# Kernel optimization log

Hardware: AMD Instinct MI355X
Metric: run time of the kernel (lower is better)

Reference implementation:

```python
import jax, jax.numpy as jnp
import numpy as np

SLOPE = 0.01

def leaky_tanh(x):
    return jnp.tanh(x * (2.0 / 3.0)) * 1.7159 + x * SLOPE

def lstm_cell(x, h, c, w_ih, w_hh, b_ih, b_hh):
    # torch LSTMCell gate order: i, f, g, o
    gates = x @ w_ih.T + b_ih + h @ w_hh.T + b_hh
    i, f, g, o = jnp.split(gates, 4, axis=-1)
    c_new = jax.nn.sigmoid(f) * c + jax.nn.sigmoid(i) * jnp.tanh(g)
    h_new = jax.nn.sigmoid(o) * jnp.tanh(c_new)
    return h_new, c_new

def setup_inputs() -> dict:
    key = jax.random.key(0)
    ks = jax.random.split(key, 16)
    T, B, I, H, O = 512, 64, 128, 2048, 64
    H1, H2 = H // 2, H // 8  # 1024, 256
    F2 = H // 4              # 512
    s = 0.02
    return {
        "inputs": jax.random.normal(ks[0], (T, B, I), dtype=jnp.float32),
        "fc1_w": jax.random.normal(ks[1], (H, I), dtype=jnp.float32) * s,
        "fc1_b": jax.random.normal(ks[2], (H,), dtype=jnp.float32) * s,
        "w_ih1": jax.random.normal(ks[3], (4 * H1, H), dtype=jnp.float32) * s,
        "w_hh1": jax.random.normal(ks[4], (4 * H1, H1), dtype=jnp.float32) * s,
        "b_ih1": jax.random.normal(ks[5], (4 * H1,), dtype=jnp.float32) * s,
        "b_hh1": jax.random.normal(ks[6], (4 * H1,), dtype=jnp.float32) * s,
        "fc2_w": jax.random.normal(ks[7], (F2, H1), dtype=jnp.float32) * s,
        "fc2_b": jax.random.normal(ks[8], (F2,), dtype=jnp.float32) * s,
        "w_ih2": jax.random.normal(ks[9], (4 * H2, F2), dtype=jnp.float32) * s,
        "w_hh2": jax.random.normal(ks[10], (4 * H2, H2), dtype=jnp.float32) * s,
        "b_ih2": jax.random.normal(ks[11], (4 * H2,), dtype=jnp.float32) * s,
        "b_hh2": jax.random.normal(ks[12], (4 * H2,), dtype=jnp.float32) * s,
        "fc3_w": jax.random.normal(ks[13], (O, H2), dtype=jnp.float32) * s,
        "fc3_b": jax.random.normal(ks[14], (O,), dtype=jnp.float32) * s,
    }

def reference(inputs, fc1_w, fc1_b, w_ih1, w_hh1, b_ih1, b_hh1,
              fc2_w, fc2_b, w_ih2, w_hh2, b_ih2, b_hh2, fc3_w, fc3_b):
    T, B, _ = inputs.shape
    H1 = w_hh1.shape[1]
    H2 = w_hh2.shape[1]
    h1 = jnp.zeros((B, H1), dtype=inputs.dtype)
    c1 = jnp.zeros((B, H1), dtype=inputs.dtype)
    h2 = jnp.zeros((B, H2), dtype=inputs.dtype)
    c2 = jnp.zeros((B, H2), dtype=inputs.dtype)

    def step(carry, xt):
        h1, c1, h2, c2 = carry
        x = leaky_tanh(xt @ fc1_w.T + fc1_b)
        h1, c1 = lstm_cell(x, h1, c1, w_ih1, w_hh1, b_ih1, b_hh1)
        x = leaky_tanh(h1 @ fc2_w.T + fc2_b)
        h2, c2 = lstm_cell(x, h2, c2, w_ih2, w_hh2, b_ih2, b_hh2)
        yhat = h2 @ fc3_w.T + fc3_b
        return (h1, c1, h2, c2), yhat

    _, outputs = jax.lax.scan(step, (h1, c1, h2, c2), inputs)
    return outputs  # [T, B, output_size]
```

## Files before the change

kernel.cpp:

```cpp
#include <hip/hip_runtime.h>
#include <hip/hip_bf16.h>

static constexpr int T_  = 512;
static constexpr int B_  = 64;
static constexpr int I_  = 128;
static constexpr int H_  = 2048;
static constexpr int H1_ = 1024;
static constexpr int F2_ = 512;
static constexpr int H2_ = 256;
static constexpr int O_  = 64;
static constexpr int G1N = 4096;
static constexpr int G2N = 1024;
static constexpr int NW  = 176;

typedef __attribute__((ext_vector_type(8))) __bf16 bfx8;
typedef __attribute__((ext_vector_type(4))) __bf16 bfx4;
typedef __attribute__((ext_vector_type(4))) float  fx4;

#define DEV __device__ __forceinline__

DEV fx4 mfma16(bfx8 a, bfx8 b, fx4 c) {
  return __builtin_amdgcn_mfma_f32_16x16x32_bf16(a, b, c, 0, 0, 0);
}
DEV float fast_sig(float x) { return 1.0f / (1.0f + __expf(-x)); }
DEV float fast_tanh(float x) {
  x = fminf(fmaxf(x, -30.0f), 30.0f);
  return 2.0f / (1.0f + __expf(-2.0f * x)) - 1.0f;
}
DEV float leaky_tanh_(float x) { return fast_tanh(x * (2.0f / 3.0f)) * 1.7159f + 0.01f * x; }

DEV void gld16c(const void* g, void* l) {
  __builtin_amdgcn_global_load_lds(
      (const __attribute__((address_space(1))) unsigned int*)g,
      (__attribute__((address_space(3))) unsigned int*)l, 16, 0, 17);
}
DEV void spin_ge(int* p, int tgt) {
  while (__hip_atomic_load(p, __ATOMIC_RELAXED, __HIP_MEMORY_SCOPE_AGENT) < tgt)
    __builtin_amdgcn_s_sleep(1);
}
DEV void stc2(unsigned short* p, unsigned short v) {
  __hip_atomic_store(p, v, __ATOMIC_RELAXED, __HIP_MEMORY_SCOPE_AGENT);
}
DEV unsigned long long ldc8(const void* p) {
  return __hip_atomic_load((const unsigned long long*)p, __ATOMIC_RELAXED,
                           __HIP_MEMORY_SCOPE_AGENT);
}
DEV unsigned short bf16bits(float f) {
  __bf16 h = (__bf16)f;
  return __builtin_bit_cast(unsigned short, h);
}
DEV void arrive1(int* p) {
  __hip_atomic_fetch_add(p, 1, __ATOMIC_RELAXED, __HIP_MEMORY_SCOPE_AGENT);
}

__global__ void k_f2b(const float* __restrict__ s, __bf16* __restrict__ d, int n4) {
  int i = blockIdx.x * blockDim.x + threadIdx.x;
  int st = gridDim.x * blockDim.x;
  for (; i < n4; i += st) {
    float4 v = ((const float4*)s)[i];
    bfx4 o = { (__bf16)v.x, (__bf16)v.y, (__bf16)v.z, (__bf16)v.w };
    ((bfx4*)d)[i] = o;
  }
}
__global__ void k_add2(const float* __restrict__ a, const float* __restrict__ b,
                       float* __restrict__ d, int n) {
  int i = blockIdx.x * blockDim.x + threadIdx.x;
  if (i < n) d[i] = a[i] + b[i];
}

__global__ void k_wre1(const float* __restrict__ w, __bf16* __restrict__ W2) {
  int v = blockIdx.x * 256 + threadIdx.x;
  int l = v & 63, kk = (v >> 6) & 31, g = (v >> 11) & 3, ng = v >> 13;
  int row = g * 1024 + ng * 16 + (l & 15);
  int k0  = kk * 32 + (l >> 4) * 8;
  const float* sp = w + (size_t)row * 1024 + k0;
  float4 v0 = ((const float4*)sp)[0];
  float4 v1 = ((const float4*)sp)[1];
  bfx8 o = { (__bf16)v0.x, (__bf16)v0.y, (__bf16)v0.z, (__bf16)v0.w,
             (__bf16)v1.x, (__bf16)v1.y, (__bf16)v1.z, (__bf16)v1.w };
  *(bfx8*)(W2 + (size_t)v * 8) = o;
}

DEV void gemm_tile(char* sm, const __bf16* __restrict__ A, const __bf16* __restrict__ W,
                   __bf16* __restrict__ outB, const float* __restrict__ bias,
                   int m0, int n0, int N, int K, int epi, int wt)
{
  __bf16 (*As)[32] = (__bf16 (*)[32])sm;
  __bf16 (*Ws)[32] = (__bf16 (*)[32])(sm + 8192);
  const int tid = threadIdx.x, lane = tid & 63, wave = tid >> 6;
  const int wm = wave >> 1, wn = wave & 1;
  const int r1 = tid >> 2, c1v = (tid & 3) * 8;
  const int kr = (lane >> 4) * 8, rr = lane & 15;
  fx4 acc[4][4] = {};
  for (int k0 = 0; k0 < K; k0 += 32) {
    __syncthreads();
    *(bfx8*)&As[r1][c1v]      = *(const bfx8*)&A[(size_t)(m0 + r1) * K + k0 + c1v];
    *(bfx8*)&As[r1 + 64][c1v] = *(const bfx8*)&A[(size_t)(m0 + r1 + 64) * K + k0 + c1v];
    *(bfx8*)&Ws[r1][c1v]      = *(const bfx8*)&W[(size_t)(n0 + r1) * K + k0 + c1v];
    *(bfx8*)&Ws[r1 + 64][c1v] = *(const bfx8*)&W[(size_t)(n0 + r1 + 64) * K + k0 + c1v];
    __syncthreads();
    bfx8 a[4], b[4];
#pragma unroll
    for (int mi = 0; mi < 4; ++mi) a[mi] = *(const bfx8*)&As[wm*64 + mi*16 + rr][kr];
#pragma unroll
    for (int ni = 0; ni < 4; ++ni) b[ni] = *(const bfx8*)&Ws[wn*64 + ni*16 + rr][kr];
#pragma unroll
    for (int mi = 0; mi < 4; ++mi)
#pragma unroll
      for (int ni = 0; ni < 4; ++ni)
        acc[mi][ni] = mfma16(a[mi], b[ni], acc[mi][ni]);
  }
  const int cr = (lane >> 4) * 4, cc = lane & 15;
#pragma unroll
  for (int mi = 0; mi < 4; ++mi)
#pragma unroll
    for (int ni = 0; ni < 4; ++ni) {
      int col = n0 + wn*64 + ni*16 + cc;
#pragma unroll
      for (int r = 0; r < 4; ++r) {
        int row = m0 + wm*64 + mi*16 + cr + r;
        float v = acc[mi][ni][r] + bias[col];
        if (epi == 1) v = leaky_tanh_(v);
        if (wt) stc2((unsigned short*)outB + ((size_t)row * N + col), bf16bits(v));
        else    outB[(size_t)row * N + col] = (__bf16)v;
      }
    }
}

__launch_bounds__(256)
__global__ void k_gemm(const __bf16* __restrict__ A, const __bf16* __restrict__ W,
                       __bf16* __restrict__ outB, const float* __restrict__ bias,
                       int M, int N, int K, int epi)
{
  __shared__ __align__(16) char sm[16384];
  (void)M;
  gemm_tile(sm, A, W, outB, bias, blockIdx.y * 128, blockIdx.x * 128, N, K, epi, 0);
}

DEV void stage(char* dst, int rsB, const __bf16* __restrict__ src, size_t sStride,
               int n, int lg) {
  for (int idx = threadIdx.x; idx < n; idx += 256) {
    int r = idx >> lg, c = idx & ((1 << lg) - 1);
    *(bfx8*)(dst + r * rsB + ((c * 16) ^ ((r & 7) << 4))) =
        *(const bfx8*)(src + (size_t)r * sStride + c * 8);
  }
}

struct KP {
  const __bf16 *W2, *whh2b;
  const __bf16 *g1rd;  __bf16 *g1wr;
  const __bf16 *xcrd;  __bf16 *xcwr;
  const __bf16 *infc1;
  const __bf16 *h1rd;  const __bf16 *h1s0;  __bf16 *h1wr;
  __bf16 *x2c; __bf16 *g2;
  const __bf16 *wfc1, *wih1, *wfc2, *wih2;
  const float *bfc1, *bs1, *bfc2, *bs2;
  float *c1, *c2;
  __bf16 *h2a;
  int *cnt;
  int Tc, t2base, do_l1, do_l2, do_fc2, do_ih1, do_fc1;
};

__launch_bounds__(256, 1)
__global__ void k_persist3(KP p)
{
  __shared__ __align__(16) char smem[131072];
  const int tid = threadIdx.x, lane = tid & 63, wv = tid >> 6;
  const int rr = lane & 15, hi = lane >> 4;
  const int col = tid & 15, brow = tid >> 4;
  const int bid = blockIdx.x;
  int* cnt = p.cnt;
  const int Tc = p.Tc;

  if (bid < 64) {
    if (!p.do_l1) return;
    const int ng = bid;
    char* As = smem;
    float* Cp = (float*)smem;

    bfx8 wreg[4][8];
#pragma unroll
    for (int g = 0; g < 4; ++g)
#pragma unroll
      for (int j = 0; j < 8; ++j)
        wreg[g][j] = *(const bfx8*)(p.W2 + (size_t)((ng * 4 + g) * 32 + wv * 8 + j) * 512 + lane * 8);

    float pc[4];
#pragma unroll
    for (int q = 0; q < 4; ++q)
      pc[q] = p.c1[(brow + q * 16) * 1024 + ng * 16 + col];

    for (int s = 0; s < Tc; ++s) {
      float pg[4][4];
#pragma unroll
      for (int q = 0; q < 4; ++q)
#pragma unroll
        for (int g = 0; g < 4; ++g)
          pg[q][g] = (float)p.g1rd[(size_t)(s * 64 + brow + q * 16) * 4096 + g * 1024 + ng * 16 + col];

      if (s > 0 && tid < 4) spin_ge(cnt + tid * 128, 16 * s);
      __syncthreads();

      const __bf16* h1s = (s == 0) ? p.h1s0 : (p.h1wr + (size_t)s * 65536);
      {
        char* dstb = smem + wv * 32768;
#pragma unroll 8
        for (int i = 0; i < 32; ++i) {
          int d = wv * 2048 + i * 64 + lane;
          int r = d >> 7;
          int sg = (r << 7) | ((d & 127) ^ (r & 7));
          gld16c(h1s + (size_t)sg * 8, dstb + i * 1024);
        }
      }
      __syncthreads();

      fx4 acc[4][4] = {};
#pragma unroll
      for (int j = 0; j < 8; ++j) {
        const int kB = (wv * 8 + j) * 64 + hi * 16;
        bfx8 a[4];
#pragma unroll
        for (int m = 0; m < 4; ++m) {
          int ra = m * 16 + rr;
          a[m] = *(const bfx8*)(As + ra * 2048 + (kB ^ ((ra & 7) << 4)));
        }
#pragma unroll
        for (int g = 0; g < 4; ++g)
#pragma unroll
          for (int m = 0; m < 4; ++m)
            acc[g][m] = mfma16(a[m], wreg[g][j], acc[g][m]);
      }
      __syncthreads();
#pragma unroll
      for (int g = 0; g < 4; ++g)
#pragma unroll
        for (int m = 0; m < 4; ++m) {
          int gc = g * 16 + rr;
          int bx = (m * 16 + hi * 4) ^ ((gc & 15) << 2);
          *(fx4*)(Cp + ((wv * 64 + gc) * 64 + bx)) = acc[g][m];
        }
      __syncthreads();

      __bf16* h1o = p.h1wr + (size_t)(s + 1) * 65536;
#pragma unroll
      for (int q = 0; q < 4; ++q) {
        int b_ = brow + q * 16;
        float gv[4];
#pragma unroll
        for (int g = 0; g < 4; ++g) {
          int gc = g * 16 + col;
          int bx = b_ ^ ((gc & 15) << 2);
          float v = pg[q][g];
#pragma unroll
          for (int w = 0; w < 4; ++w)
            v += Cp[(w * 64 + gc) * 64 + bx];
          gv[g] = v;
        }
        float cn = fast_sig(gv[1]) * pc[q] + fast_sig(gv[0]) * fast_tanh(gv[2]);
        pc[q] = cn;
        float hv = fast_sig(gv[3]) * fast_tanh(cn);
        stc2((unsigned short*)h1o + (b_ * 1024 + ng * 16 + col), bf16bits(hv));
      }
      __syncthreads();
      if (tid == 0) arrive1(cnt + (ng & 3) * 128);
    }
#pragma unroll
    for (int q = 0; q < 4; ++q)
      p.c1[(brow + q * 16) * 1024 + ng * 16 + col] = pc[q];

  } else if (bid < 80) {
    if (!p.do_l2) return;
    const int ng2 = bid - 64;
    char* Ws2 = smem;
    char* As2 = smem + 32768;
    float (*Gx2)[64][16] = (float (*)[64][16])(smem + 32768);

    for (int idx = tid; idx < 2048; idx += 256) {
      int r = idx >> 5, c = idx & 31;
      int wr = (r >> 4) * 256 + ng2 * 16 + (r & 15);
      *(bfx8*)(Ws2 + r * 512 + ((c * 16) ^ ((r & 7) << 4))) =
          *(const bfx8*)(p.whh2b + (size_t)wr * 256 + c * 8);
    }
    float pc2[4];
#pragma unroll
    for (int q = 0; q < 4; ++q)
      pc2[q] = p.c2[(brow + q * 16) * 256 + ng2 * 16 + col];

    if (tid == 0) spin_ge(cnt + 640, NW);
    __syncthreads();

    for (int s = 0; s < Tc; ++s) {
      float pg[4][4];
#pragma unroll
      for (int q = 0; q < 4; ++q)
#pragma unroll
        for (int g = 0; g < 4; ++g)
          pg[q][g] = (float)p.g2[(size_t)(s * 64 + brow + q * 16) * 1024 + g * 256 + ng2 * 16 + col];

      if (s > 0 && tid == 0) spin_ge(cnt + 512, 16 * s);
      __syncthreads();

      const __bf16* h2s = p.h2a + (size_t)(p.t2base + s) * 16384;
      for (int idx = tid; idx < 2048; idx += 256) {
        int r = idx >> 5, c = idx & 31;
        const char* sp = (const char*)(h2s + r * 256 + c * 8);
        unsigned long long lo = ldc8(sp), hi8 = ldc8(sp + 8);
        char* dp = As2 + r * 512 + ((c * 16) ^ ((r & 7) << 4));
        *(unsigned long long*)dp = lo;
        *(unsigned long long*)(dp + 8) = hi8;
      }
      __syncthreads();

      fx4 acc[4] = {};
#pragma unroll
      for (int ks = 0; ks < 8; ++ks) {
        const int cb = ks * 64 + hi * 16;
        int rb = wv * 16 + rr;
        bfx8 bfr = *(const bfx8*)(Ws2 + rb * 512 + (cb ^ ((rb & 7) << 4)));
#pragma unroll
        for (int m = 0; m < 4; ++m) {
          int ra = m * 16 + rr;
          bfx8 afr = *(const bfx8*)(As2 + ra * 512 + (cb ^ ((ra & 7) << 4)));
          acc[m] = mfma16(afr, bfr, acc[m]);
        }
      }
      __syncthreads();
#pragma unroll
      for (int m = 0; m < 4; ++m)
#pragma unroll
        for (int r = 0; r < 4; ++r)
          Gx2[wv][m * 16 + hi * 4 + r][rr] = acc[m][r];
      __syncthreads();

      __bf16* h2o = p.h2a + (size_t)(p.t2base + s + 1) * 16384;
#pragma unroll
      for (int q = 0; q < 4; ++q) {
        int b_ = brow + q * 16;
        float gi = Gx2[0][b_][col] + pg[q][0];
        float gf = Gx2[1][b_][col] + pg[q][1];
        float gg = Gx2[2][b_][col] + pg[q][2];
        float go = Gx2[3][b_][col] + pg[q][3];
        float cn = fast_sig(gf) * pc2[q] + fast_sig(gi) * fast_tanh(gg);
        pc2[q] = cn;
        float hv = fast_sig(go) * fast_tanh(cn);
        stc2((unsigned short*)h2o + (b_ * 256 + ng2 * 16 + col), bf16bits(hv));
      }
      __syncthreads();
      if (tid == 0) arrive1(cnt + 512);
    }
#pragma unroll
    for (int q = 0; q < 4; ++q)
      p.c2[(brow + q * 16) * 256 + ng2 * 16 + col] = pc2[q];

  } else {
    const int wid = bid - 80;
    const int Mt = (Tc * 64) / 128;
    if (p.do_fc2) {
      for (int i = wid; i < Mt * 4; i += NW)
        gemm_tile(smem, p.h1rd + 65536, p.wfc2, p.x2c, p.bfc2,
                  (i >> 2) * 128, (i & 3) * 128, F2_, H1_, 1, 1);
      __syncthreads();
      if (tid == 0) { arrive1(cnt + 576); spin_ge(cnt + 576, NW); }
      __syncthreads();
      for (int i = wid; i < Mt * 8; i += NW)
        gemm_tile(smem, p.x2c, p.wih2, p.g2, p.bs2,
                  (i >> 3) * 128, (i & 7) * 128, G2N, F2_, 0, 1);
      __syncthreads();
      if (tid == 0) arrive1(cnt + 640);
    }
    if (p.do_ih1) {
      for (int i = wid; i < Mt * 32; i += NW)
        gemm_tile(smem, p.xcrd, p.wih1, p.g1wr, p.bs1,
                  (i >> 5) * 128, (i & 31) * 128, G1N, H_, 0, 0);
    }
    if (p.do_fc1) {
      for (int i = wid; i < Mt * 16; i += NW)
        gemm_tile(smem, p.infc1, p.wfc1, p.xcwr, p.bfc1,
                  (i >> 4) * 128, (i & 15) * 128, H_, I_, 1, 0);
    }
  }
}

__launch_bounds__(256)
__global__ void k_fc3b(const __bf16* __restrict__ H2mat, const __bf16* __restrict__ w3,
                       const float* __restrict__ b3, float* __restrict__ out)
{
  __shared__ __align__(16) char smem[65536];
  const int tid = threadIdx.x, lane = tid & 63, wv = tid >> 6;
  const int rr = lane & 15, hi = lane >> 4;
  char* As = smem;
  char* Ws = smem + 32768;
  const size_t row0 = (size_t)blockIdx.x * 64;
  stage(As, 512, H2mat + row0 * 256, 256, 2048, 5);
  stage(Ws, 512, w3, 256, 2048, 5);
  __syncthreads();
  fx4 acc[4] = {};
#pragma unroll
  for (int ks = 0; ks < 8; ++ks) {
    const int cbB = ks * 64 + hi * 16;
    int rb = wv * 16 + rr;
    bfx8 bfr = *(const bfx8*)(Ws + rb * 512 + (cbB ^ ((rb & 7) << 4)));
#pragma unroll
    for (int m = 0; m < 4; ++m) {
      int ra = m * 16 + rr;
      bfx8 afr = *(const bfx8*)(As + ra * 512 + (cbB ^ ((ra & 7) << 4)));
      acc[m] = mfma16(afr, bfr, acc[m]);
    }
  }
  float bv = b3[wv * 16 + rr];
#pragma unroll
  for (int m = 0; m < 4; ++m)
#pragma unroll
    for (int r = 0; r < 4; ++r)
      out[(row0 + m * 16 + hi * 4 + r) * 64 + wv * 16 + rr] = acc[m][r] + bv;
}

extern "C" void kernel_launch(void* const* d_in, const int* in_sizes, int n_in,
                              void* d_out, int out_size, void* d_ws, size_t ws_size,
                              hipStream_t stream)
{
  (void)in_sizes; (void)n_in; (void)out_size;
  const float* f_in = (const float*)d_in[0];
  const float* fc1w = (const float*)d_in[1];
  const float* fc1b = (const float*)d_in[2];
  const float* wih1 = (const float*)d_in[3];
  const float* whh1 = (const float*)d_in[4];
  const float* bih1 = (const float*)d_in[5];
  const float* bhh1 = (const float*)d_in[6];
  const float* fc2w = (const float*)d_in[7];
  const float* fc2b = (const float*)d_in[8];
  const float* wih2 = (const float*)d_in[9];
  const float* whh2 = (const float*)d_in[10];
  const float* bih2 = (const float*)d_in[11];
  const float* bhh2 = (const float*)d_in[12];
  const float* fc3w = (const float*)d_in[13];
  const float* fc3b = (const float*)d_in[14];
  float* out = (float*)d_out;

  char* base = (char*)d_ws;
  size_t off = 0;
  auto alloc = [&](size_t bytes) -> char* {
    char* q = base + off;
    off = (off + bytes + 255) & ~(size_t)255;
    return q;
  };
  __bf16* wb_fc1 = (__bf16*)alloc((size_t)H_ * I_ * 2);
  __bf16* wb_ih1 = (__bf16*)alloc((size_t)G1N * H_ * 2);
  __bf16* W2     = (__bf16*)alloc((size_t)G1N * H1_ * 2);
  __bf16* wb_fc2 = (__bf16*)alloc((size_t)F2_ * H1_ * 2);
  __bf16* wb_ih2 = (__bf16*)alloc((size_t)G2N * F2_ * 2);
  __bf16* wb_hh2 = (__bf16*)alloc((size_t)G2N * H2_ * 2);
  __bf16* wb_fc3 = (__bf16*)alloc((size_t)O_ * H2_ * 2);
  __bf16* in_bf  = (__bf16*)alloc((size_t)T_ * B_ * I_ * 2);
  float*  bsum1  = (float*) alloc((size_t)G1N * 4);
  float*  bsum2  = (float*) alloc((size_t)G2N * 4);
  float*  c1     = (float*) alloc((size_t)B_ * H1_ * 4);
  float*  c2     = (float*) alloc((size_t)B_ * H2_ * 4);
  __bf16* h2a    = (__bf16*)alloc((size_t)(T_ + 1) * B_ * H2_ * 2);
  __bf16* h1zero = (__bf16*)alloc((size_t)B_ * H1_ * 2);
  int*    cnt    = (int*)   alloc(4096);
  size_t fixed = off;

  auto perTc = [](size_t Tc) -> size_t {
    size_t Mc = Tc * 64;
    return 2 * Mc * H_ * 2
         + 2 * Mc * G1N * 2
         + 2 * (Tc + 1) * (size_t)B_ * H1_ * 2
         + Mc * F2_ * 2
         + Mc * G2N * 2
         + 10 * 256;
  };
  int Tc = 128;
  while (Tc > 2 && fixed + perTc(Tc) > ws_size) Tc >>= 1;
  const int Mc = Tc * 64;
  __bf16* XcA  = (__bf16*)alloc((size_t)Mc * H_ * 2);
  __bf16* XcB  = (__bf16*)alloc((size_t)Mc * H_ * 2);
  __bf16* G1A  = (__bf16*)alloc((size_t)Mc * G1N * 2);
  __bf16* G1B  = (__bf16*)alloc((size_t)Mc * G1N * 2);
  __bf16* h1rA = (__bf16*)alloc((size_t)(Tc + 1) * B_ * H1_ * 2);
  __bf16* h1rB = (__bf16*)alloc((size_t)(Tc + 1) * B_ * H1_ * 2);
  __bf16* x2c  = (__bf16*)alloc((size_t)Mc * F2_ * 2);
  __bf16* G2cb = (__bf16*)alloc((size_t)Mc * G2N * 2);

  struct CV { const float* s; __bf16* d; int n; } cvs[7] = {
    {fc1w, wb_fc1, H_ * I_},   {wih1, wb_ih1, G1N * H_},
    {fc2w, wb_fc2, F2_ * H1_}, {wih2, wb_ih2, G2N * F2_}, {whh2, wb_hh2, G2N * H2_},
    {fc3w, wb_fc3, O_ * H2_},  {f_in, in_bf, T_ * B_ * I_},
  };
  for (int i = 0; i < 7; ++i) {
    int n4 = cvs[i].n / 4;
    int blocks = (n4 + 255) / 256;
    if (blocks > 2048) blocks = 2048;
    k_f2b<<<blocks, 256, 0, stream>>>(cvs[i].s, cvs[i].d, n4);
  }
  k_wre1<<<2048, 256, 0, stream>>>(whh1, W2);
  k_add2<<<G1N / 256, 256, 0, stream>>>(bih1, bhh1, bsum1, G1N);
  k_add2<<<G2N / 256, 256, 0, stream>>>(bih2, bhh2, bsum2, G2N);
  hipMemsetAsync(c1, 0, (size_t)B_ * H1_ * 4, stream);
  hipMemsetAsync(c2, 0, (size_t)B_ * H2_ * 4, stream);
  hipMemsetAsync(h1zero, 0, (size_t)B_ * H1_ * 2, stream);
  hipMemsetAsync(h2a, 0, (size_t)B_ * H2_ * 2, stream);

  const int chunks = T_ / Tc;
  k_gemm<<<dim3(H_ / 128, Mc / 128), 256, 0, stream>>>(in_bf, wb_fc1, XcA, fc1b, Mc, H_, I_, 1);
  k_gemm<<<dim3(G1N / 128, Mc / 128), 256, 0, stream>>>(XcA, wb_ih1, G1A, bsum1, Mc, G1N, H_, 0);
  if (chunks > 1)
    k_gemm<<<dim3(H_ / 128, Mc / 128), 256, 0, stream>>>(
        in_bf + (size_t)Mc * I_, wb_fc1, XcB, fc1b, Mc, H_, I_, 1);

  KP p;
  p.W2 = W2; p.whh2b = wb_hh2;
  p.wfc1 = wb_fc1; p.wih1 = wb_ih1; p.wfc2 = wb_fc2; p.wih2 = wb_ih2;
  p.bfc1 = fc1b; p.bs1 = bsum1; p.bfc2 = fc2b; p.bs2 = bsum2;
  p.c1 = c1; p.c2 = c2; p.h2a = h2a; p.cnt = cnt;
  p.x2c = x2c; p.g2 = G2cb; p.Tc = Tc;

  for (int k = 0; k < chunks; ++k) {
    hipMemsetAsync(cnt, 0, 4096, stream);
    p.g1rd = (k & 1) ? G1B : G1A;
    p.g1wr = (k & 1) ? G1A : G1B;
    p.xcrd = ((k + 1) & 1) ? XcB : XcA;
    p.xcwr = (k & 1) ? XcB : XcA;
    p.infc1 = (k + 2 < chunks) ? (in_bf + (size_t)(k + 2) * Mc * I_) : in_bf;
    p.h1wr = (k & 1) ? h1rB : h1rA;
    p.h1rd = (k & 1) ? h1rA : h1rB;
    p.h1s0 = (k == 0) ? h1zero : (p.h1rd + (size_t)Tc * 65536);
    p.t2base = (k - 1) * Tc;
    p.do_l1 = 1;
    p.do_l2 = (k >= 1);
    p.do_fc2 = (k >= 1);
    p.do_ih1 = (k + 1 < chunks);
    p.do_fc1 = (k + 2 < chunks);
    k_persist3<<<256, 256, 0, stream>>>(p);
  }
  hipMemsetAsync(cnt, 0, 4096, stream);
  p.h1rd = ((chunks - 1) & 1) ? h1rB : h1rA;
  p.h1wr = p.h1rd == h1rA ? h1rB : h1rA;
  p.h1s0 = h1zero;
  p.g1rd = G1A; p.g1wr = G1B; p.xcrd = XcA; p.xcwr = XcB; p.infc1 = in_bf;
  p.t2base = (chunks - 1) * Tc;
  p.do_l1 = 0; p.do_l2 = 1; p.do_fc2 = 1; p.do_ih1 = 0; p.do_fc1 = 0;
  k_persist3<<<256, 256, 0, stream>>>(p);
  k_fc3b<<<(T_ * B_) / 64, 256, 0, stream>>>(h2a + (size_t)B_ * H2_, wb_fc3, fc3b, out);
}
```

Baseline: 3.445 ms.

## Pipeline layer-2 within the same chunk via fine-grained counters and dynamic work pool

Layer 2 (fc2, ih2 GEMMs and the LSTM2 recurrence) now runs in the same persistent launch as layer 1. It consumes h1 two timesteps at a time through per-row-block counters, which removes the one-chunk lag and the extra tail launch. Layer-1 blocks now wait per wave on the per-quarter h1 counter and do their own LDS loads without block-wide barriers. The generic GEMM tile moves to K=64 steps with async global-to-LDS loads and an XOR swizzle. The ih1/fc1 prefetch GEMMs are handed out through an atomic work queue. This adds more spin-wait points and counter traffic, and correctness depends on the counter targets being right.

```diff
diff --git a/kernel.cpp b/kernel.cpp
--- a/kernel.cpp
+++ b/kernel.cpp
@@ -12,6 +12,7 @@
 static constexpr int G1N = 4096;
 static constexpr int G2N = 1024;
 static constexpr int NW  = 176;
+static constexpr int NCH = 48;
 
 typedef __attribute__((ext_vector_type(8))) __bf16 bfx8;
 typedef __attribute__((ext_vector_type(4))) __bf16 bfx4;
@@ -29,6 +30,11 @@
 }
 DEV float leaky_tanh_(float x) { return fast_tanh(x * (2.0f / 3.0f)) * 1.7159f + 0.01f * x; }
 
+DEV void gld16(const void* g, void* l) {
+  __builtin_amdgcn_global_load_lds(
+      (const __attribute__((address_space(1))) unsigned int*)g,
+      (__attribute__((address_space(3))) unsigned int*)l, 16, 0, 0);
+}
 DEV void gld16c(const void* g, void* l) {
   __builtin_amdgcn_global_load_lds(
       (const __attribute__((address_space(1))) unsigned int*)g,
@@ -52,6 +58,12 @@
 DEV void arrive1(int* p) {
   __hip_atomic_fetch_add(p, 1, __ATOMIC_RELAXED, __HIP_MEMORY_SCOPE_AGENT);
 }
+
+#define C_H1(w)  ((w) * 32)
+#define C_H2     128
+#define C_FC2(r) (256 + (r) * 16)
+#define C_G2(r)  (1536 + (r) * 16)
+#define C_POOL   2816
 
 __global__ void k_f2b(const float* __restrict__ s, __bf16* __restrict__ d, int n4) {
   int i = blockIdx.x * blockDim.x + threadIdx.x;
@@ -85,40 +97,52 @@
                    __bf16* __restrict__ outB, const float* __restrict__ bias,
                    int m0, int n0, int N, int K, int epi, int wt)
 {
-  __bf16 (*As)[32] = (__bf16 (*)[32])sm;
-  __bf16 (*Ws)[32] = (__bf16 (*)[32])(sm + 8192);
+  char* As = sm;
+  char* Ws = sm + 16384;
   const int tid = threadIdx.x, lane = tid & 63, wave = tid >> 6;
   const int wm = wave >> 1, wn = wave & 1;
-  const int r1 = tid >> 2, c1v = (tid & 3) * 8;
-  const int kr = (lane >> 4) * 8, rr = lane & 15;
+  const int rr = lane & 15, hi = lane >> 4;
   fx4 acc[4][4] = {};
-  for (int k0 = 0; k0 < K; k0 += 32) {
+  for (int k0 = 0; k0 < K; k0 += 64) {
     __syncthreads();
-    *(bfx8*)&As[r1][c1v]      = *(const bfx8*)&A[(size_t)(m0 + r1) * K + k0 + c1v];
-    *(bfx8*)&As[r1 + 64][c1v] = *(const bfx8*)&A[(size_t)(m0 + r1 + 64) * K + k0 + c1v];
-    *(bfx8*)&Ws[r1][c1v]      = *(const bfx8*)&W[(size_t)(n0 + r1) * K + k0 + c1v];
-    *(bfx8*)&Ws[r1 + 64][c1v] = *(const bfx8*)&W[(size_t)(n0 + r1 + 64) * K + k0 + c1v];
+#pragma unroll
+    for (int i = 0; i < 4; ++i) {
+      int idx = i * 256 + tid;
+      int r = idx >> 3, cs = (idx & 7) ^ (r & 7);
+      gld16(A + (size_t)(m0 + r) * K + k0 + cs * 8, As + idx * 16);
+      gld16(W + (size_t)(n0 + r) * K + k0 + cs * 8, Ws + idx * 16);
+    }
     __syncthreads();
-    bfx8 a[4], b[4];
-#pragma unroll
-    for (int mi = 0; mi < 4; ++mi) a[mi] = *(const bfx8*)&As[wm*64 + mi*16 + rr][kr];
-#pragma unroll
-    for (int ni = 0; ni < 4; ++ni) b[ni] = *(const bfx8*)&Ws[wn*64 + ni*16 + rr][kr];
-#pragma unroll
-    for (int mi = 0; mi < 4; ++mi)
-#pragma unroll
-      for (int ni = 0; ni < 4; ++ni)
-        acc[mi][ni] = mfma16(a[mi], b[ni], acc[mi][ni]);
-  }
-  const int cr = (lane >> 4) * 4, cc = lane & 15;
+#pragma unroll
+    for (int kh = 0; kh < 2; ++kh) {
+      bfx8 a[4], b[4];
+      const int cg = kh * 4 + hi;
+#pragma unroll
+      for (int mi = 0; mi < 4; ++mi) {
+        int ra = wm * 64 + mi * 16 + rr;
+        a[mi] = *(const bfx8*)(As + ra * 128 + ((cg ^ (ra & 7)) << 4));
+      }
+#pragma unroll
+      for (int ni = 0; ni < 4; ++ni) {
+        int rb = wn * 64 + ni * 16 + rr;
+        b[ni] = *(const bfx8*)(Ws + rb * 128 + ((cg ^ (rb & 7)) << 4));
+      }
+#pragma unroll
+      for (int mi = 0; mi < 4; ++mi)
+#pragma unroll
+        for (int ni = 0; ni < 4; ++ni)
+          acc[mi][ni] = mfma16(a[mi], b[ni], acc[mi][ni]);
+    }
+  }
+  const int cr = hi * 4, cc = rr;
 #pragma unroll
   for (int mi = 0; mi < 4; ++mi)
 #pragma unroll
     for (int ni = 0; ni < 4; ++ni) {
-      int col = n0 + wn*64 + ni*16 + cc;
+      int col = n0 + wn * 64 + ni * 16 + cc;
 #pragma unroll
       for (int r = 0; r < 4; ++r) {
-        int row = m0 + wm*64 + mi*16 + cr + r;
+        int row = m0 + wm * 64 + mi * 16 + cr + r;
         float v = acc[mi][ni][r] + bias[col];
         if (epi == 1) v = leaky_tanh_(v);
         if (wt) stc2((unsigned short*)outB + ((size_t)row * N + col), bf16bits(v));
@@ -132,7 +156,7 @@
                        __bf16* __restrict__ outB, const float* __restrict__ bias,
                        int M, int N, int K, int epi)
 {
-  __shared__ __align__(16) char sm[16384];
+  __shared__ __align__(16) char sm[32768];
   (void)M;
   gemm_tile(sm, A, W, outB, bias, blockIdx.y * 128, blockIdx.x * 128, N, K, epi, 0);
 }
@@ -151,18 +175,18 @@
   const __bf16 *g1rd;  __bf16 *g1wr;
   const __bf16 *xcrd;  __bf16 *xcwr;
   const __bf16 *infc1;
-  const __bf16 *h1rd;  const __bf16 *h1s0;  __bf16 *h1wr;
+  const __bf16 *h1s0;  __bf16 *h1wr;
   __bf16 *x2c; __bf16 *g2;
   const __bf16 *wfc1, *wih1, *wfc2, *wih2;
   const float *bfc1, *bs1, *bfc2, *bs2;
   float *c1, *c2;
   __bf16 *h2a;
   int *cnt;
-  int Tc, t2base, do_l1, do_l2, do_fc2, do_ih1, do_fc1;
+  int Tc, t2base, do_ih1, do_fc1;
 };
 
 __launch_bounds__(256, 1)
-__global__ void k_persist3(KP p)
+__global__ void k_persist4(KP p)
 {
   __shared__ __align__(16) char smem[131072];
   const int tid = threadIdx.x, lane = tid & 63, wv = tid >> 6;
@@ -173,10 +197,9 @@
   const int Tc = p.Tc;
 
   if (bid < 64) {
-    if (!p.do_l1) return;
     const int ng = bid;
-    char* As = smem;
     float* Cp = (float*)smem;
+    char* As_w = smem + wv * 32768;
 
     bfx8 wreg[4][8];
 #pragma unroll
@@ -198,31 +221,29 @@
         for (int g = 0; g < 4; ++g)
           pg[q][g] = (float)p.g1rd[(size_t)(s * 64 + brow + q * 16) * 4096 + g * 1024 + ng * 16 + col];
 
-      if (s > 0 && tid < 4) spin_ge(cnt + tid * 128, 16 * s);
-      __syncthreads();
+      if (s > 0 && lane == 0) spin_ge(cnt + C_H1(wv), 16 * s);
 
       const __bf16* h1s = (s == 0) ? p.h1s0 : (p.h1wr + (size_t)s * 65536);
-      {
-        char* dstb = smem + wv * 32768;
 #pragma unroll 8
-        for (int i = 0; i < 32; ++i) {
-          int d = wv * 2048 + i * 64 + lane;
-          int r = d >> 7;
-          int sg = (r << 7) | ((d & 127) ^ (r & 7));
-          gld16c(h1s + (size_t)sg * 8, dstb + i * 1024);
-        }
-      }
-      __syncthreads();
+      for (int i = 0; i < 32; ++i) {
+        int idx = i * 64 + lane;
+        int r = idx >> 5, cg = idx & 31;
+        int sg = r * 128 + wv * 32 + (cg ^ (r & 7));
+        gld16c(h1s + (size_t)sg * 8, As_w + i * 1024);
+      }
+      __builtin_amdgcn_sched_barrier(0);
+      asm volatile("s_waitcnt vmcnt(0)" ::: "memory");
+      __builtin_amdgcn_sched_barrier(0);
 
       fx4 acc[4][4] = {};
 #pragma unroll
       for (int j = 0; j < 8; ++j) {
-        const int kB = (wv * 8 + j) * 64 + hi * 16;
+        const int cg = j * 4 + hi;
         bfx8 a[4];
 #pragma unroll
         for (int m = 0; m < 4; ++m) {
           int ra = m * 16 + rr;
-          a[m] = *(const bfx8*)(As + ra * 2048 + (kB ^ ((ra & 7) << 4)));
+          a[m] = *(const bfx8*)(As_w + ra * 512 + ((cg ^ (ra & 7)) << 4));
         }
 #pragma unroll
         for (int g = 0; g < 4; ++g)
@@ -262,14 +283,13 @@
         stc2((unsigned short*)h1o + (b_ * 1024 + ng * 16 + col), bf16bits(hv));
       }
       __syncthreads();
-      if (tid == 0) arrive1(cnt + (ng & 3) * 128);
+      if (tid == 0) arrive1(cnt + C_H1(ng >> 4));
     }
 #pragma unroll
     for (int q = 0; q < 4; ++q)
       p.c1[(brow + q * 16) * 1024 + ng * 16 + col] = pc[q];
 
   } else if (bid < 80) {
-    if (!p.do_l2) return;
     const int ng2 = bid - 64;
     char* Ws2 = smem;
     char* As2 = smem + 32768;
@@ -285,20 +305,21 @@
 #pragma unroll
     for (int q = 0; q < 4; ++q)
       pc2[q] = p.c2[(brow + q * 16) * 256 + ng2 * 16 + col];
-
-    if (tid == 0) spin_ge(cnt + 640, NW);
     __syncthreads();
 
     for (int s = 0; s < Tc; ++s) {
+      if (tid == 0) {
+        spin_ge(cnt + C_G2(s >> 1), 8);
+        if (s > 0) spin_ge(cnt + C_H2, 16 * s);
+      }
+      __syncthreads();
+
       float pg[4][4];
 #pragma unroll
       for (int q = 0; q < 4; ++q)
 #pragma unroll
         for (int g = 0; g < 4; ++g)
           pg[q][g] = (float)p.g2[(size_t)(s * 64 + brow + q * 16) * 1024 + g * 256 + ng2 * 16 + col];
-
-      if (s > 0 && tid == 0) spin_ge(cnt + 512, 16 * s);
-      __syncthreads();
 
       const __bf16* h2s = p.h2a + (size_t)(p.t2base + s) * 16384;
       for (int idx = tid; idx < 2048; idx += 256) {
@@ -346,7 +367,7 @@
         stc2((unsigned short*)h2o + (b_ * 256 + ng2 * 16 + col), bf16bits(hv));
       }
       __syncthreads();
-      if (tid == 0) arrive1(cnt + 512);
+      if (tid == 0) arrive1(cnt + C_H2);
     }
 #pragma unroll
     for (int q = 0; q < 4; ++q)
@@ -354,29 +375,51 @@
 
   } else {
     const int wid = bid - 80;
-    const int Mt = (Tc * 64) / 128;
-    if (p.do_fc2) {
-      for (int i = wid; i < Mt * 4; i += NW)
-        gemm_tile(smem, p.h1rd + 65536, p.wfc2, p.x2c, p.bfc2,
-                  (i >> 2) * 128, (i & 3) * 128, F2_, H1_, 1, 1);
-      __syncthreads();
-      if (tid == 0) { arrive1(cnt + 576); spin_ge(cnt + 576, NW); }
-      __syncthreads();
-      for (int i = wid; i < Mt * 8; i += NW)
-        gemm_tile(smem, p.x2c, p.wih2, p.g2, p.bs2,
-                  (i >> 3) * 128, (i & 7) * 128, G2N, F2_, 0, 1);
-      __syncthreads();
-      if (tid == 0) arrive1(cnt + 640);
-    }
-    if (p.do_ih1) {
-      for (int i = wid; i < Mt * 32; i += NW)
+    const int NRB = Tc >> 1;
+    if (wid < NCH) {
+      for (int t = wid; t < NRB * 4; t += NCH) {
+        int rb = t >> 2, n = t & 3;
+        if (tid == 0) {
+          spin_ge(cnt + C_H1(0), 16 * (2 * rb + 2));
+          spin_ge(cnt + C_H1(1), 16 * (2 * rb + 2));
+          spin_ge(cnt + C_H1(2), 16 * (2 * rb + 2));
+          spin_ge(cnt + C_H1(3), 16 * (2 * rb + 2));
+        }
+        __syncthreads();
+        gemm_tile(smem, p.h1wr + (size_t)(2 * rb + 1) * 65536, p.wfc2,
+                  p.x2c + (size_t)rb * 128 * F2_, p.bfc2, 0, n * 128, F2_, H1_, 1, 1);
+        __syncthreads();
+        if (tid == 0) arrive1(cnt + C_FC2(rb));
+      }
+      for (int t = wid; t < NRB * 8; t += NCH) {
+        int rb = t >> 3, n = t & 7;
+        if (tid == 0) spin_ge(cnt + C_FC2(rb), 4);
+        __syncthreads();
+        gemm_tile(smem, p.x2c + (size_t)rb * 128 * F2_, p.wih2,
+                  p.g2 + (size_t)rb * 128 * G2N, p.bs2, 0, n * 128, G2N, F2_, 0, 1);
+        __syncthreads();
+        if (tid == 0) arrive1(cnt + C_G2(rb));
+      }
+    }
+    const int nih = p.do_ih1 ? NRB * 32 : 0;
+    const int nfc = p.do_fc1 ? NRB * 16 : 0;
+    if (nih + nfc == 0) return;
+    __shared__ int tsh;
+    while (true) {
+      if (tid == 0)
+        tsh = __hip_atomic_fetch_add(cnt + C_POOL, 1, __ATOMIC_RELAXED,
+                                     __HIP_MEMORY_SCOPE_AGENT);
+      __syncthreads();
+      int t = tsh;
+      if (t < nih) {
         gemm_tile(smem, p.xcrd, p.wih1, p.g1wr, p.bs1,
-                  (i >> 5) * 128, (i & 31) * 128, G1N, H_, 0, 0);
-    }
-    if (p.do_fc1) {
-      for (int i = wid; i < Mt * 16; i += NW)
+                  (t >> 5) * 128, (t & 31) * 128, G1N, H_, 0, 0);
+      } else if (t < nih + nfc) {
+        int t2 = t - nih;
         gemm_tile(smem, p.infc1, p.wfc1, p.xcwr, p.bfc1,
-                  (i >> 4) * 128, (i & 15) * 128, H_, I_, 1, 0);
+                  (t2 >> 4) * 128, (t2 & 15) * 128, H_, I_, 1, 0);
+      } else break;
+      __syncthreads();
     }
   }
 }
@@ -458,17 +501,14 @@
   float*  c2     = (float*) alloc((size_t)B_ * H2_ * 4);
   __bf16* h2a    = (__bf16*)alloc((size_t)(T_ + 1) * B_ * H2_ * 2);
   __bf16* h1zero = (__bf16*)alloc((size_t)B_ * H1_ * 2);
-  int*    cnt    = (int*)   alloc(4096);
+  int*    cnt    = (int*)   alloc(16384);
   size_t fixed = off;
 
   auto perTc = [](size_t Tc) -> size_t {
     size_t Mc = Tc * 64;
-    return 2 * Mc * H_ * 2
-         + 2 * Mc * G1N * 2
+    return 2 * Mc * H_ * 2 + 2 * Mc * G1N * 2
          + 2 * (Tc + 1) * (size_t)B_ * H1_ * 2
-         + Mc * F2_ * 2
-         + Mc * G2N * 2
-         + 10 * 256;
+         + Mc * F2_ * 2 + Mc * G2N * 2 + 10 * 256;
   };
   int Tc = 128;
   while (Tc > 2 && fixed + perTc(Tc) > ws_size) Tc >>= 1;
@@ -516,30 +556,19 @@
   p.x2c = x2c; p.g2 = G2cb; p.Tc = Tc;
 
   for (int k = 0; k < chunks; ++k) {
-    hipMemsetAsync(cnt, 0, 4096, stream);
+    hipMemsetAsync(cnt, 0, 16384, stream);
     p.g1rd = (k & 1) ? G1B : G1A;
     p.g1wr = (k & 1) ? G1A : G1B;
     p.xcrd = ((k + 1) & 1) ? XcB : XcA;
     p.xcwr = (k & 1) ? XcB : XcA;
     p.infc1 = (k + 2 < chunks) ? (in_bf + (size_t)(k + 2) * Mc * I_) : in_bf;
     p.h1wr = (k & 1) ? h1rB : h1rA;
-    p.h1rd = (k & 1) ? h1rA : h1rB;
-    p.h1s0 = (k == 0) ? h1zero : (p.h1rd + (size_t)Tc * 65536);
-    p.t2base = (k - 1) * Tc;
-    p.do_l1 = 1;
-    p.do_l2 = (k >= 1);
-    p.do_fc2 = (k >= 1);
+    const __bf16* h1prev = (k & 1) ? h1rA : h1rB;
+    p.h1s0 = (k == 0) ? h1zero : (h1prev + (size_t)Tc * 65536);
+    p.t2base = k * Tc;
     p.do_ih1 = (k + 1 < chunks);
     p.do_fc1 = (k + 2 < chunks);
-    k_persist3<<<256, 256, 0, stream>>>(p);
-  }
-  hipMemsetAsync(cnt, 0, 4096, stream);
-  p.h1rd = ((chunks - 1) & 1) ? h1rB : h1rA;
-  p.h1wr = p.h1rd == h1rA ? h1rB : h1rA;
-  p.h1s0 = h1zero;
-  p.g1rd = G1A; p.g1wr = G1B; p.xcrd = XcA; p.xcwr = XcB; p.infc1 = in_bf;
-  p.t2base = (chunks - 1) * Tc;
-  p.do_l1 = 0; p.do_l2 = 1; p.do_fc2 = 1; p.do_ih1 = 0; p.do_fc1 = 0;
-  k_persist3<<<256, 256, 0, stream>>>(p);
+    k_persist4<<<256, 256, 0, stream>>>(p);
+  }
   k_fc3b<<<(T_ * B_) / 64, 256, 0, stream>>>(h2a + (size_t)B_ * H2_, wb_fc3, fc3b, out);
 }
```

Result: slower. 5.558 ms (+61.3%).

## Use direct global-to-LDS loads with XOR swizzle and BK=64 in GEMM tile

Applied to the files above, without the earlier changes.

Rewrites the shared GEMM tile so operand tiles are loaded straight from global memory into LDS via global_load_lds, with an XOR-swizzled 128-byte row layout to avoid bank conflicts. The K step grows from 32 to 64, halving the number of barrier pairs per tile, and the shared-memory buffer doubles to 32 KB. This aims to cut register round-trips and synchronization overhead in the non-recurrent GEMMs, which are a small part of the total runtime dominated by the recurrent persistent kernel. gemm_tile may also be called from the persistent kernel with a smaller sm buffer, which is a consistency risk.

```diff
diff --git a/kernel.cpp b/kernel.cpp
--- a/kernel.cpp
+++ b/kernel.cpp
@@ -29,6 +29,11 @@
 }
 DEV float leaky_tanh_(float x) { return fast_tanh(x * (2.0f / 3.0f)) * 1.7159f + 0.01f * x; }
 
+DEV void gld16(const void* g, void* l) {
+  __builtin_amdgcn_global_load_lds(
+      (const __attribute__((address_space(1))) unsigned int*)g,
+      (__attribute__((address_space(3))) unsigned int*)l, 16, 0, 0);
+}
 DEV void gld16c(const void* g, void* l) {
   __builtin_amdgcn_global_load_lds(
       (const __attribute__((address_space(1))) unsigned int*)g,
@@ -85,40 +90,52 @@
                    __bf16* __restrict__ outB, const float* __restrict__ bias,
                    int m0, int n0, int N, int K, int epi, int wt)
 {
-  __bf16 (*As)[32] = (__bf16 (*)[32])sm;
-  __bf16 (*Ws)[32] = (__bf16 (*)[32])(sm + 8192);
+  char* As = sm;
+  char* Ws = sm + 16384;
   const int tid = threadIdx.x, lane = tid & 63, wave = tid >> 6;
   const int wm = wave >> 1, wn = wave & 1;
-  const int r1 = tid >> 2, c1v = (tid & 3) * 8;
-  const int kr = (lane >> 4) * 8, rr = lane & 15;
+  const int rr = lane & 15, hi = lane >> 4;
   fx4 acc[4][4] = {};
-  for (int k0 = 0; k0 < K; k0 += 32) {
+  for (int k0 = 0; k0 < K; k0 += 64) {
     __syncthreads();
-    *(bfx8*)&As[r1][c1v]      = *(const bfx8*)&A[(size_t)(m0 + r1) * K + k0 + c1v];
-    *(bfx8*)&As[r1 + 64][c1v] = *(const bfx8*)&A[(size_t)(m0 + r1 + 64) * K + k0 + c1v];
-    *(bfx8*)&Ws[r1][c1v]      = *(const bfx8*)&W[(size_t)(n0 + r1) * K + k0 + c1v];
-    *(bfx8*)&Ws[r1 + 64][c1v] = *(const bfx8*)&W[(size_t)(n0 + r1 + 64) * K + k0 + c1v];
+#pragma unroll
+    for (int i = 0; i < 4; ++i) {
+      int idx = i * 256 + tid;
+      int r = idx >> 3, cs = (idx & 7) ^ (r & 7);
+      gld16(A + (size_t)(m0 + r) * K + k0 + cs * 8, As + idx * 16);
+      gld16(W + (size_t)(n0 + r) * K + k0 + cs * 8, Ws + idx * 16);
+    }
     __syncthreads();
-    bfx8 a[4], b[4];
-#pragma unroll
-    for (int mi = 0; mi < 4; ++mi) a[mi] = *(const bfx8*)&As[wm*64 + mi*16 + rr][kr];
-#pragma unroll
-    for (int ni = 0; ni < 4; ++ni) b[ni] = *(const bfx8*)&Ws[wn*64 + ni*16 + rr][kr];
-#pragma unroll
-    for (int mi = 0; mi < 4; ++mi)
-#pragma unroll
-      for (int ni = 0; ni < 4; ++ni)
-        acc[mi][ni] = mfma16(a[mi], b[ni], acc[mi][ni]);
-  }
-  const int cr = (lane >> 4) * 4, cc = lane & 15;
+#pragma unroll
+    for (int kh = 0; kh < 2; ++kh) {
+      bfx8 a[4], b[4];
+      const int cg = kh * 4 + hi;
+#pragma unroll
+      for (int mi = 0; mi < 4; ++mi) {
+        int ra = wm * 64 + mi * 16 + rr;
+        a[mi] = *(const bfx8*)(As + ra * 128 + ((cg ^ (ra & 7)) << 4));
+      }
+#pragma unroll
+      for (int ni = 0; ni < 4; ++ni) {
+        int rb = wn * 64 + ni * 16 + rr;
+        b[ni] = *(const bfx8*)(Ws + rb * 128 + ((cg ^ (rb & 7)) << 4));
+      }
+#pragma unroll
+      for (int mi = 0; mi < 4; ++mi)
+#pragma unroll
+        for (int ni = 0; ni < 4; ++ni)
+          acc[mi][ni] = mfma16(a[mi], b[ni], acc[mi][ni]);
+    }
+  }
+  const int cr = hi * 4, cc = rr;
 #pragma unroll
   for (int mi = 0; mi < 4; ++mi)
 #pragma unroll
     for (int ni = 0; ni < 4; ++ni) {
-      int col = n0 + wn*64 + ni*16 + cc;
+      int col = n0 + wn * 64 + ni * 16 + cc;
 #pragma unroll
       for (int r = 0; r < 4; ++r) {
-        int row = m0 + wm*64 + mi*16 + cr + r;
+        int row = m0 + wm * 64 + mi * 16 + cr + r;
         float v = acc[mi][ni][r] + bias[col];
         if (epi == 1) v = leaky_tanh_(v);
         if (wt) stc2((unsigned short*)outB + ((size_t)row * N + col), bf16bits(v));
@@ -132,7 +149,7 @@
                        __bf16* __restrict__ outB, const float* __restrict__ bias,
                        int M, int N, int K, int epi)
 {
-  __shared__ __align__(16) char sm[16384];
+  __shared__ __align__(16) char sm[32768];
   (void)M;
   gemm_tile(sm, A, W, outB, bias, blockIdx.y * 128, blockIdx.x * 128, N, K, epi, 0);
 }
```

Result: faster. 3.350 ms (-2.8%).
